# Kernel optimization log

Measured on AMD Instinct MI355X. Metric: run time of the kernel, lower is better.

Reference implementation:

```python
import jax, jax.numpy as jnp
import numpy as np

ALPHA = 0.8   # dice-score exponent
BETA = 0.2    # class-prob exponent
EPS = 1e-4    # dice denominator epsilon (SparseInst dice_score)


def _hungarian_max(cost):
    """Rectangular linear_sum_assignment(maximize=True) for a numpy (n,m) cost.
    Pads to square, runs the O(s^3) Hungarian algorithm with potentials.
    Returns (rows, cols) of length min(n,m), rows sorted (matches scipy)."""
    n, m = cost.shape
    s = max(n, m)
    c = np.zeros((s, s), dtype=np.float64)
    c[:n, :m] = -cost  # maximize -> minimize
    INF = 1e18
    u = np.zeros(s + 1)
    v = np.zeros(s + 1)
    p = np.zeros(s + 1, dtype=np.int64)
    way = np.zeros(s + 1, dtype=np.int64)
    for i in range(1, s + 1):
        p[0] = i
        j0 = 0
        minv = np.full(s + 1, INF)
        used = np.zeros(s + 1, dtype=bool)
        while True:
            used[j0] = True
            i0 = p[j0]
            cur = c[i0 - 1, :] - u[i0] - v[1:]
            free = ~used[1:]
            upd = free & (cur < minv[1:])
            minv[1:][upd] = cur[upd]
            way[1:][upd] = j0
            cand = np.where(free, minv[1:], INF)
            j1 = int(np.argmin(cand)) + 1
            delta = cand[j1 - 1]
            u[p[used]] += delta
            v[used] -= delta
            minv[~used] -= delta
            j0 = j1
            if p[j0] == 0:
                break
        while j0:
            j1 = way[j0]
            p[j0] = p[j1]
            j0 = j1
    rows, cols = [], []
    for j in range(1, s + 1):
        i = p[j]
        if i - 1 < n and j - 1 < m:
            rows.append(i - 1)
            cols.append(j - 1)
    order = np.argsort(np.asarray(rows))
    return np.asarray(rows)[order], np.asarray(cols)[order]


def _cost_matrix(pred_masks, pred_logits, tgt_masks, tgt_ids):
    B, N, H, W = pred_masks.shape
    T = tgt_masks.shape[0]
    pm = jax.nn.sigmoid(pred_masks.astype(jnp.float32)).reshape(B * N, H * W)
    # bilinear resize (align_corners=False / half-pixel) of GT masks to pred grid
    tm = jax.image.resize(tgt_masks.astype(jnp.float32), (T, H, W), method='linear')
    tm = tm.reshape(T, H * W)
    # dice score: 2<p,t> / (|p|^2 + |t|^2 + eps)   -> (B*N, T)
    num = 2.0 * jnp.einsum('qd,td->qt', pm, tm)
    den = jnp.sum(pm * pm, axis=-1)[:, None] + jnp.sum(tm * tm, axis=-1)[None, :]
    dice = num / (den + EPS)
    prob = jax.nn.sigmoid(pred_logits.astype(jnp.float32)).reshape(B * N, -1)[:, tgt_ids]
    C = dice ** ALPHA * prob ** BETA
    return C.reshape(B, N, T)


_cost_matrix_jit = jax.jit(_cost_matrix)


def setup_inputs() -> dict:
    key = jax.random.key(0)
    k1, k2, k3, k4 = jax.random.split(key, 4)
    B, N, H, W = 16, 100, 128, 128
    T, NC = 320, 80
    return {
        'pred_masks': jax.random.normal(k1, (B, N, H, W), dtype=jnp.float32),
        'pred_logits': jax.random.normal(k2, (B, N, NC), dtype=jnp.float32),
        'tgt_masks': jax.random.uniform(k3, (T, 2 * H, 2 * W), dtype=jnp.float32),
        'tgt_ids': jax.random.randint(k4, (T,), 0, NC, dtype=jnp.int64) if jax.config.jax_enable_x64 else jax.random.randint(k4, (T,), 0, NC, dtype=jnp.int32),
    }


def reference(pred_masks, pred_logits, tgt_masks, tgt_ids):
    B, N = pred_masks.shape[:2]
    T = tgt_masks.shape[0]
    per_img = T // B  # uniform sizes per image (stands in for [len(v['masks'])])
    C = _cost_matrix_jit(pred_masks, pred_logits, tgt_masks, tgt_ids)
    Cn = np.asarray(jax.device_get(C))
    rows, cols = [], []
    for b in range(B):
        r, c = _hungarian_max(Cn[b, :, b * per_img:(b + 1) * per_img])
        rows.append(r)
        cols.append(c)
    rows = jnp.asarray(np.stack(rows), dtype=jnp.int32)  # (B, per_img)
    cols = jnp.asarray(np.stack(cols), dtype=jnp.int32)  # (B, per_img)
    return C, rows, cols
```

## Files before the change

kernel.cpp:

```cpp
#include <hip/hip_runtime.h>
#include <math.h>

#define NB 16
#define NP 100
#define NT 320
#define NCLS 80
#define WO 128
#define HW 16384
#define QT 1600
#define PI 20
#define KSPLIT 8
#define KSLICE 2048
#define BK 32
#define KTILES 64
#define SRC_W 256
#define BM 32
#define BN 320
#define CH 16

typedef _Float16 half2v __attribute__((ext_vector_type(2)));
typedef _Float16 half4v __attribute__((ext_vector_type(4)));
typedef _Float16 half8v __attribute__((ext_vector_type(8)));
typedef float f32x4 __attribute__((ext_vector_type(4)));

#define GLOAD_LDS16(gp, lp) __builtin_amdgcn_global_load_lds(                         \
    (const __attribute__((address_space(1))) void*)(gp),                              \
    (__attribute__((address_space(3))) void*)(lp), 16, 0, 0)

#define SWZ(r) (((r) & 3) ^ (((r) >> 2) & 3))

__device__ __forceinline__ float sigf(float x){ return 1.0f/(1.0f+expf(-x)); }
__device__ __forceinline__ float sigfast(float x){ return 1.0f/(1.0f+__expf(-x)); }

__device__ __forceinline__ void mkw128(int i, float* w, int* ix){
  int j0 = 2*i - 1;
  ix[0]=j0; ix[1]=j0+1; ix[2]=j0+2; ix[3]=j0+3;
  w[0]=0.125f; w[1]=0.375f; w[2]=0.375f; w[3]=0.125f;
  if (i == 0){ ix[0]=0; w[0]=0.0f; w[1]=3.0f/7.0f; w[2]=3.0f/7.0f; w[3]=1.0f/7.0f; }
  if (i == 127){ ix[3]=255; w[3]=0.0f; w[0]=1.0f/7.0f; w[1]=3.0f/7.0f; w[2]=3.0f/7.0f; }
}

__global__ __launch_bounds__(256) void k_downsample(const float* __restrict__ tgt,
                                                    _Float16* __restrict__ tm,
                                                    float* __restrict__ tqpart){
  const int blk = blockIdx.x;
  const int t = blk >> 3;
  const int c = blk & 7;
  const int x = threadIdx.x;
  const int oy0 = c * CH;
  const int r0 = 2*oy0 - 1;
  const float* src = tgt + (size_t)t * (SRC_W*SRC_W);
  __shared__ float vbuf[CH][SRC_W];
  __shared__ float wred[4];

  float cc[34];
  #pragma unroll
  for (int li = 0; li < 34; ++li){
    int r = r0 + li; r = r < 0 ? 0 : (r > 255 ? 255 : r);
    cc[li] = src[r*SRC_W + x];
  }
  #pragma unroll
  for (int dy = 0; dy < CH; ++dy){
    int oy = oy0 + dy;
    float w0=0.125f, w1=0.375f, w2=0.375f, w3=0.125f;
    if (oy == 0){ w0=0.0f; w1=3.0f/7.0f; w2=3.0f/7.0f; w3=1.0f/7.0f; }
    if (oy == 127){ w3=0.0f; w0=1.0f/7.0f; w1=3.0f/7.0f; w2=3.0f/7.0f; }
    vbuf[dy][x] = w0*cc[2*dy] + w1*cc[2*dy+1] + w2*cc[2*dy+2] + w3*cc[2*dy+3];
  }
  __syncthreads();

  float ssq = 0.f;
  _Float16* dst = tm + (size_t)t * HW + (size_t)oy0 * WO;
  #pragma unroll
  for (int i = 0; i < 8; ++i){
    int e = x + 256*i;
    int oy = e >> 7;
    int ox = e & 127;
    float w[4]; int ix[4];
    mkw128(ox, w, ix);
    float val = w[0]*vbuf[oy][ix[0]] + w[1]*vbuf[oy][ix[1]]
              + w[2]*vbuf[oy][ix[2]] + w[3]*vbuf[oy][ix[3]];
    dst[oy*WO + ox] = (_Float16)val;
    ssq += val*val;
  }
  for (int off=32; off; off>>=1) ssq += __shfl_xor(ssq, off);
  if ((x & 63) == 0) wred[x >> 6] = ssq;
  __syncthreads();
  if (x == 0) tqpart[c*NT + t] = wred[0]+wred[1]+wred[2]+wred[3];
}

__global__ __launch_bounds__(512) void k_gemm(const float* __restrict__ A,
                                              const _Float16* __restrict__ Bm,
                                              float* __restrict__ part,
                                              float* __restrict__ pqpart){
  __shared__ _Float16 As[2][BM*BK];
  __shared__ _Float16 Bs[2][BN*BK];
  const int tid = threadIdx.x;
  const int lane = tid & 63;
  const int wid = tid >> 6;
  const int wr = wid & 1;
  const int wc = wid >> 1;
  const int id = blockIdx.x;
  const int z = id & 7;
  const int q0 = (id >> 3) * BM;
  const int ks = z * KSLICE;

  const int ar = tid >> 4;
  const int acg = tid & 15;
  const float* ap = A + (size_t)(q0 + ar) * HW + ks + acg*2;
  const int awoff = ar*BK + ((acg >> 2) ^ SWZ(ar))*8 + (acg & 3)*2;

  f32x4 acc[5];
  #pragma unroll
  for (int n = 0; n < 5; ++n) acc[n] = (f32x4){0.f,0.f,0.f,0.f};
  float pqs = 0.f;

  #pragma unroll
  for (int i = 0; i < 3; ++i){
    int g = i*512 + tid;
    if (g < 1280){
      int row = g >> 2, slot = g & 3;
      const _Float16* gp = Bm + (size_t)row*HW + ks + (slot ^ SWZ(row))*8;
      GLOAD_LDS16(gp, &Bs[0][(size_t)g*8]);
    }
  }
  {
    float2 a0 = *(const float2*)ap;
    float s0 = sigfast(a0.x), s1 = sigfast(a0.y);
    pqs += s0*s0 + s1*s1;
    half2v hh = { (_Float16)s0, (_Float16)s1 };
    *(half2v*)&As[0][awoff] = hh;
  }
  __syncthreads();

  for (int kt = 0; kt < KTILES; ++kt){
    const int cur = kt & 1, nxt = cur ^ 1;
    float2 a;
    if (kt + 1 < KTILES){
      #pragma unroll
      for (int i = 0; i < 3; ++i){
        int g = i*512 + tid;
        if (g < 1280){
          int row = g >> 2, slot = g & 3;
          const _Float16* gp = Bm + (size_t)row*HW + ks + (kt+1)*BK + (slot ^ SWZ(row))*8;
          GLOAD_LDS16(gp, &Bs[nxt][(size_t)g*8]);
        }
      }
      a = *(const float2*)(ap + (kt+1)*BK);
    }
    half8v af, bf[5];
    {
      int r = wr*16 + (lane & 15);
      af = *(const half8v*)&As[cur][r*BK + (((lane>>4) ^ SWZ(r)))*8];
    }
    #pragma unroll
    for (int n = 0; n < 5; ++n){
      int r = wc*80 + n*16 + (lane & 15);
      bf[n] = *(const half8v*)&Bs[cur][r*BK + (((lane>>4) ^ SWZ(r)))*8];
    }
    #pragma unroll
    for (int n = 0; n < 5; ++n)
      acc[n] = __builtin_amdgcn_mfma_f32_16x16x32_f16(af, bf[n], acc[n], 0, 0, 0);
    if (kt + 1 < KTILES){
      float s0 = sigfast(a.x), s1 = sigfast(a.y);
      pqs += s0*s0 + s1*s1;
      half2v hh = { (_Float16)s0, (_Float16)s1 };
      *(half2v*)&As[nxt][awoff] = hh;
    }
    __syncthreads();
  }

  float* op = part + (size_t)z * (QT*NT);
  {
    int qb = q0 + wr*16 + (lane >> 4)*4;
    #pragma unroll
    for (int n = 0; n < 5; ++n){
      int t = wc*80 + n*16 + (lane & 15);
      #pragma unroll
      for (int r = 0; r < 4; ++r)
        op[(size_t)(qb + r)*NT + t] = acc[n][r];
    }
  }
  pqs += __shfl_xor(pqs, 1);
  pqs += __shfl_xor(pqs, 2);
  pqs += __shfl_xor(pqs, 4);
  pqs += __shfl_xor(pqs, 8);
  if ((tid & 15) == 0) pqpart[z*QT + q0 + ar] = pqs;
}

__global__ __launch_bounds__(256) void k_cost(const float* __restrict__ part,
                                              const float* __restrict__ pqpart,
                                              const float* __restrict__ tqpart,
                                              const float* __restrict__ logits,
                                              const int* __restrict__ ids,
                                              float* __restrict__ Cout){
  int idx = blockIdx.x * 256 + threadIdx.x;
  int q = idx / NT;
  int t = idx - q * NT;
  float num = 0.f;
  #pragma unroll
  for (int s = 0; s < KSPLIT; ++s) num += part[(size_t)s * (QT*NT) + idx];
  num *= 2.0f;
  float pqv = 0.f;
  #pragma unroll
  for (int s = 0; s < KSPLIT; ++s) pqv += pqpart[s * QT + q];
  float tqv = 0.f;
  #pragma unroll
  for (int s = 0; s < 8; ++s) tqv += tqpart[s * NT + t];
  float den = pqv + tqv + 1e-4f;
  float dice = num / den;
  float prob = sigf(logits[q * NCLS + ids[t]]);
  Cout[idx] = powf(dice, 0.8f) * powf(prob, 0.2f);
}

__global__ __launch_bounds__(64) void k_hung(const float* __restrict__ C,
                                             float* __restrict__ rows_out,
                                             float* __restrict__ cols_out){
  const int b = blockIdx.x;
  const int lane = threadIdx.x;
  __shared__ float negC[PI*NP];
  __shared__ double u[PI+1];
  __shared__ int p[NP+1];
  __shared__ int way[NP+1];
  for (int e = lane; e < PI*NP; e += 64){
    int i = e / NP, j = e - i*NP;
    negC[e] = -C[(size_t)(b*NP + j)*NT + (b*PI + i)];
  }
  if (lane <= PI) u[lane] = 0.0;
  for (int j = lane; j <= NP; j += 64){ p[j] = 0; way[j] = 0; }
  __syncthreads();
  const int jA = lane + 1;
  const int jB = lane + 65;
  const bool hasB = (jB <= NP);
  double vA = 0.0, vB = 0.0;
  const double INFD = 1e18;
  for (int i = 1; i <= PI; ++i){
    if (lane == 0) p[0] = i;
    __syncthreads();
    double mvA = INFD, mvB = INFD;
    bool usA = false, usB = false;
    int j0 = 0;
    int jbrk = 0;
    while (true){
      if (jA == j0) usA = true;
      if (hasB && jB == j0) usB = true;
      int i0 = p[j0];
      double ui0 = u[i0];
      double candA = INFD, candB = INFD;
      if (!usA){
        double cur = (double)negC[(i0-1)*NP + (jA-1)] - ui0 - vA;
        if (cur < mvA){ mvA = cur; way[jA] = j0; }
        candA = mvA;
      }
      if (hasB && !usB){
        double cur = (double)negC[(i0-1)*NP + (jB-1)] - ui0 - vB;
        if (cur < mvB){ mvB = cur; way[jB] = j0; }
        candB = mvB;
      }
      double bv; int bj;
      if (candB < candA){ bv = candB; bj = jB; } else { bv = candA; bj = jA; }
      for (int off = 32; off; off >>= 1){
        double ov = __shfl_xor(bv, off);
        int oj = __shfl_xor(bj, off);
        if (ov < bv || (ov == bv && oj < bj)){ bv = ov; bj = oj; }
      }
      const double delta = bv;
      if (usA){ int pj = p[jA]; u[pj] += delta; vA -= delta; }
      else mvA -= delta;
      if (hasB){
        if (usB){ int pj = p[jB]; u[pj] += delta; vB -= delta; }
        else mvB -= delta;
      }
      if (lane == 0) u[p[0]] += delta;
      __syncthreads();
      j0 = bj;
      if (p[j0] == 0){ jbrk = j0; break; }
    }
    __syncthreads();
    if (lane == 0){
      int j0a = jbrk;
      while (j0a){
        int jp = way[j0a];
        p[j0a] = p[jp];
        j0a = jp;
      }
    }
    __syncthreads();
  }
  if (lane == 0){
    int cnt = 0;
    for (int j = 1; j <= NP; ++j){
      int pi = p[j];
      if (pi != 0){
        rows_out[b*PI + cnt] = (float)(j - 1);
        cols_out[b*PI + cnt] = (float)(pi - 1);
        ++cnt;
      }
    }
  }
}

extern "C" void kernel_launch(void* const* d_in, const int* in_sizes, int n_in,
                              void* d_out, int out_size, void* d_ws, size_t ws_size,
                              hipStream_t stream){
  const float* pred_masks  = (const float*)d_in[0];
  const float* pred_logits = (const float*)d_in[1];
  const float* tgt_masks   = (const float*)d_in[2];
  const int*   tgt_ids     = (const int*)d_in[3];
  float* out = (float*)d_out;
  char* ws = (char*)d_ws;
  _Float16* Th  = (_Float16*)ws;
  float* tqpart = (float*)(ws + (size_t)NT*HW*2);
  float* pqpart = (float*)(ws + (size_t)NT*HW*2 + 16384);
  float* part   = (float*)(ws + (size_t)NT*HW*2 + 16384 + 65536);

  k_downsample<<<NT*8, 256, 0, stream>>>(tgt_masks, Th, tqpart);
  k_gemm<<<50*KSPLIT, 512, 0, stream>>>(pred_masks, Th, part, pqpart);
  k_cost<<<(QT*NT)/256, 256, 0, stream>>>(part, pqpart, tqpart, pred_logits, tgt_ids, out);
  k_hung<<<NB, 64, 0, stream>>>(out, out + (size_t)QT*NT, out + (size_t)QT*NT + NT);
}
```

Measured before the change: 138.2 us.

## Load GEMM A operand directly into registers and double the K tile

```diff
diff --git a/kernel.cpp b/kernel.cpp
--- a/kernel.cpp
+++ b/kernel.cpp
@@ -11,23 +11,19 @@
 #define PI 20
 #define KSPLIT 8
 #define KSLICE 2048
-#define BK 32
-#define KTILES 64
+#define BK 64
+#define KTILES 32
 #define SRC_W 256
 #define BM 32
 #define BN 320
 #define CH 16
 
-typedef _Float16 half2v __attribute__((ext_vector_type(2)));
-typedef _Float16 half4v __attribute__((ext_vector_type(4)));
 typedef _Float16 half8v __attribute__((ext_vector_type(8)));
 typedef float f32x4 __attribute__((ext_vector_type(4)));
 
 #define GLOAD_LDS16(gp, lp) __builtin_amdgcn_global_load_lds(                         \
     (const __attribute__((address_space(1))) void*)(gp),                              \
     (__attribute__((address_space(3))) void*)(lp), 16, 0, 0)
-
-#define SWZ(r) (((r) & 3) ^ (((r) >> 2) & 3))
 
 __device__ __forceinline__ float sigf(float x){ return 1.0f/(1.0f+expf(-x)); }
 __device__ __forceinline__ float sigfast(float x){ return 1.0f/(1.0f+__expf(-x)); }
@@ -89,26 +85,22 @@
   if (x == 0) tqpart[c*NT + t] = wred[0]+wred[1]+wred[2]+wred[3];
 }
 
-__global__ __launch_bounds__(512) void k_gemm(const float* __restrict__ A,
-                                              const _Float16* __restrict__ Bm,
-                                              float* __restrict__ part,
-                                              float* __restrict__ pqpart){
-  __shared__ _Float16 As[2][BM*BK];
+__global__ __launch_bounds__(512, 3) void k_gemm(const float* __restrict__ A,
+                                                 const _Float16* __restrict__ Bm,
+                                                 float* __restrict__ part,
+                                                 float* __restrict__ pqpart){
   __shared__ _Float16 Bs[2][BN*BK];
   const int tid = threadIdx.x;
   const int lane = tid & 63;
   const int wid = tid >> 6;
-  const int wr = wid & 1;
-  const int wc = wid >> 1;
+  const int wr = wid >> 2;
+  const int wc = wid & 3;
   const int id = blockIdx.x;
   const int z = id & 7;
   const int q0 = (id >> 3) * BM;
   const int ks = z * KSLICE;
 
-  const int ar = tid >> 4;
-  const int acg = tid & 15;
-  const float* ap = A + (size_t)(q0 + ar) * HW + ks + acg*2;
-  const int awoff = ar*BK + ((acg >> 2) ^ SWZ(ar))*8 + (acg & 3)*2;
+  const float* ap = A + (size_t)(q0 + wr*16 + (lane & 15)) * HW + ks + (lane >> 4) * 8;
 
   f32x4 acc[5];
   #pragma unroll
@@ -116,58 +108,68 @@
   float pqs = 0.f;
 
   #pragma unroll
-  for (int i = 0; i < 3; ++i){
+  for (int i = 0; i < 5; ++i){
     int g = i*512 + tid;
-    if (g < 1280){
-      int row = g >> 2, slot = g & 3;
-      const _Float16* gp = Bm + (size_t)row*HW + ks + (slot ^ SWZ(row))*8;
-      GLOAD_LDS16(gp, &Bs[0][(size_t)g*8]);
-    }
-  }
-  {
-    float2 a0 = *(const float2*)ap;
-    float s0 = sigfast(a0.x), s1 = sigfast(a0.y);
-    pqs += s0*s0 + s1*s1;
-    half2v hh = { (_Float16)s0, (_Float16)s1 };
-    *(half2v*)&As[0][awoff] = hh;
-  }
-  __syncthreads();
+    int row = g >> 3, s = g & 7;
+    GLOAD_LDS16(Bm + (size_t)row*HW + ks + ((s ^ (row & 7)) * 8), &Bs[0][(size_t)g*8]);
+  }
+  float4 a0 = *(const float4*)(ap);
+  float4 a1 = *(const float4*)(ap + 4);
+  float4 a2 = *(const float4*)(ap + 32);
+  float4 a3 = *(const float4*)(ap + 36);
+  asm volatile("s_waitcnt vmcnt(0)" ::: "memory");
+  __builtin_amdgcn_s_barrier();
 
   for (int kt = 0; kt < KTILES; ++kt){
     const int cur = kt & 1, nxt = cur ^ 1;
-    float2 a;
     if (kt + 1 < KTILES){
       #pragma unroll
-      for (int i = 0; i < 3; ++i){
+      for (int i = 0; i < 5; ++i){
         int g = i*512 + tid;
-        if (g < 1280){
-          int row = g >> 2, slot = g & 3;
-          const _Float16* gp = Bm + (size_t)row*HW + ks + (kt+1)*BK + (slot ^ SWZ(row))*8;
-          GLOAD_LDS16(gp, &Bs[nxt][(size_t)g*8]);
-        }
-      }
-      a = *(const float2*)(ap + (kt+1)*BK);
-    }
-    half8v af, bf[5];
+        int row = g >> 3, s = g & 7;
+        GLOAD_LDS16(Bm + (size_t)row*HW + ks + (kt+1)*BK + ((s ^ (row & 7)) * 8),
+                    &Bs[nxt][(size_t)g*8]);
+      }
+    }
+    float4 b0, b1, b2, b3;
+    if (kt + 1 < KTILES){
+      const float* apn = ap + (kt+1)*BK;
+      b0 = *(const float4*)(apn);
+      b1 = *(const float4*)(apn + 4);
+      b2 = *(const float4*)(apn + 32);
+      b3 = *(const float4*)(apn + 36);
+    }
     {
-      int r = wr*16 + (lane & 15);
-      af = *(const half8v*)&As[cur][r*BK + (((lane>>4) ^ SWZ(r)))*8];
-    }
-    #pragma unroll
-    for (int n = 0; n < 5; ++n){
-      int r = wc*80 + n*16 + (lane & 15);
-      bf[n] = *(const half8v*)&Bs[cur][r*BK + (((lane>>4) ^ SWZ(r)))*8];
-    }
-    #pragma unroll
-    for (int n = 0; n < 5; ++n)
-      acc[n] = __builtin_amdgcn_mfma_f32_16x16x32_f16(af, bf[n], acc[n], 0, 0, 0);
-    if (kt + 1 < KTILES){
-      float s0 = sigfast(a.x), s1 = sigfast(a.y);
-      pqs += s0*s0 + s1*s1;
-      half2v hh = { (_Float16)s0, (_Float16)s1 };
-      *(half2v*)&As[nxt][awoff] = hh;
-    }
-    __syncthreads();
+      float s0 = sigfast(a0.x), s1 = sigfast(a0.y), s2 = sigfast(a0.z), s3 = sigfast(a0.w);
+      float s4 = sigfast(a1.x), s5 = sigfast(a1.y), s6 = sigfast(a1.z), s7 = sigfast(a1.w);
+      pqs += s0*s0 + s1*s1 + s2*s2 + s3*s3 + s4*s4 + s5*s5 + s6*s6 + s7*s7;
+      half8v af = { (_Float16)s0, (_Float16)s1, (_Float16)s2, (_Float16)s3,
+                    (_Float16)s4, (_Float16)s5, (_Float16)s6, (_Float16)s7 };
+      #pragma unroll
+      for (int n = 0; n < 5; ++n){
+        int r = wc*80 + n*16 + (lane & 15);
+        int s = 0*4 + (lane >> 4);
+        half8v bf = *(const half8v*)&Bs[cur][r*BK + ((s ^ (r & 7)) * 8)];
+        acc[n] = __builtin_amdgcn_mfma_f32_16x16x32_f16(af, bf, acc[n], 0, 0, 0);
+      }
+    }
+    {
+      float s0 = sigfast(a2.x), s1 = sigfast(a2.y), s2 = sigfast(a2.z), s3 = sigfast(a2.w);
+      float s4 = sigfast(a3.x), s5 = sigfast(a3.y), s6 = sigfast(a3.z), s7 = sigfast(a3.w);
+      pqs += s0*s0 + s1*s1 + s2*s2 + s3*s3 + s4*s4 + s5*s5 + s6*s6 + s7*s7;
+      half8v af = { (_Float16)s0, (_Float16)s1, (_Float16)s2, (_Float16)s3,
+                    (_Float16)s4, (_Float16)s5, (_Float16)s6, (_Float16)s7 };
+      #pragma unroll
+      for (int n = 0; n < 5; ++n){
+        int r = wc*80 + n*16 + (lane & 15);
+        int s = 1*4 + (lane >> 4);
+        half8v bf = *(const half8v*)&Bs[cur][r*BK + ((s ^ (r & 7)) * 8)];
+        acc[n] = __builtin_amdgcn_mfma_f32_16x16x32_f16(af, bf, acc[n], 0, 0, 0);
+      }
+    }
+    asm volatile("s_waitcnt vmcnt(4)" ::: "memory");
+    __builtin_amdgcn_s_barrier();
+    if (kt + 1 < KTILES){ a0 = b0; a1 = b1; a2 = b2; a3 = b3; }
   }
 
   float* op = part + (size_t)z * (QT*NT);
@@ -181,11 +183,11 @@
         op[(size_t)(qb + r)*NT + t] = acc[n][r];
     }
   }
-  pqs += __shfl_xor(pqs, 1);
-  pqs += __shfl_xor(pqs, 2);
-  pqs += __shfl_xor(pqs, 4);
-  pqs += __shfl_xor(pqs, 8);
-  if ((tid & 15) == 0) pqpart[z*QT + q0 + ar] = pqs;
+  if (wc == 0){
+    pqs += __shfl_xor(pqs, 16);
+    pqs += __shfl_xor(pqs, 32);
+    if (lane < 16) pqpart[z*QT + q0 + wr*16 + lane] = pqs;
+  }
 }
 
 __global__ __launch_bounds__(256) void k_cost(const float* __restrict__ part,
```

After: 156.0 us. 1.13x slower.

## Retile split-K GEMM to 64x160 blocks with BK=64 and deeper A prefetch

Applied to the files above, without the earlier changes.

```diff
diff --git a/kernel.cpp b/kernel.cpp
--- a/kernel.cpp
+++ b/kernel.cpp
@@ -11,23 +11,19 @@
 #define PI 20
 #define KSPLIT 8
 #define KSLICE 2048
-#define BK 32
-#define KTILES 64
+#define BK 64
+#define KTILES 32
 #define SRC_W 256
-#define BM 32
-#define BN 320
+#define BM 64
+#define BN 160
 #define CH 16
 
-typedef _Float16 half2v __attribute__((ext_vector_type(2)));
-typedef _Float16 half4v __attribute__((ext_vector_type(4)));
 typedef _Float16 half8v __attribute__((ext_vector_type(8)));
 typedef float f32x4 __attribute__((ext_vector_type(4)));
 
 #define GLOAD_LDS16(gp, lp) __builtin_amdgcn_global_load_lds(                         \
     (const __attribute__((address_space(1))) void*)(gp),                              \
     (__attribute__((address_space(3))) void*)(lp), 16, 0, 0)
-
-#define SWZ(r) (((r) & 3) ^ (((r) >> 2) & 3))
 
 __device__ __forceinline__ float sigf(float x){ return 1.0f/(1.0f+expf(-x)); }
 __device__ __forceinline__ float sigfast(float x){ return 1.0f/(1.0f+__expf(-x)); }
@@ -89,26 +85,26 @@
   if (x == 0) tqpart[c*NT + t] = wred[0]+wred[1]+wred[2]+wred[3];
 }
 
-__global__ __launch_bounds__(512) void k_gemm(const float* __restrict__ A,
-                                              const _Float16* __restrict__ Bm,
-                                              float* __restrict__ part,
-                                              float* __restrict__ pqpart){
+__global__ __launch_bounds__(512, 4) void k_gemm(const float* __restrict__ A,
+                                                 const _Float16* __restrict__ Bm,
+                                                 float* __restrict__ part,
+                                                 float* __restrict__ pqpart){
   __shared__ _Float16 As[2][BM*BK];
   __shared__ _Float16 Bs[2][BN*BK];
   const int tid = threadIdx.x;
   const int lane = tid & 63;
   const int wid = tid >> 6;
-  const int wr = wid & 1;
-  const int wc = wid >> 1;
-  const int id = blockIdx.x;
-  const int z = id & 7;
-  const int q0 = (id >> 3) * BM;
+  const int rg = wid >> 1;
+  const int cg = wid & 1;
+  const int q0 = blockIdx.x * BM;
+  const int t0 = blockIdx.y * BN;
+  const int z  = blockIdx.z;
   const int ks = z * KSLICE;
 
-  const int ar = tid >> 4;
-  const int acg = tid & 15;
-  const float* ap = A + (size_t)(q0 + ar) * HW + ks + acg*2;
-  const int awoff = ar*BK + ((acg >> 2) ^ SWZ(ar))*8 + (acg & 3)*2;
+  const int ar = tid >> 3;
+  const int ac8 = tid & 7;
+  const float* ap = A + (size_t)(q0 + ar) * HW + ks + ac8*8;
+  const int awoff = ar*BK + ((ac8 ^ (ar & 7)) * 8);
 
   f32x4 acc[5];
   #pragma unroll
@@ -119,73 +115,97 @@
   for (int i = 0; i < 3; ++i){
     int g = i*512 + tid;
     if (g < 1280){
-      int row = g >> 2, slot = g & 3;
-      const _Float16* gp = Bm + (size_t)row*HW + ks + (slot ^ SWZ(row))*8;
-      GLOAD_LDS16(gp, &Bs[0][(size_t)g*8]);
+      int row = g >> 3, s = g & 7;
+      GLOAD_LDS16(Bm + (size_t)(t0 + row)*HW + ks + ((s ^ (row & 7)) * 8),
+                  &Bs[0][(size_t)g*8]);
     }
   }
   {
-    float2 a0 = *(const float2*)ap;
-    float s0 = sigfast(a0.x), s1 = sigfast(a0.y);
-    pqs += s0*s0 + s1*s1;
-    half2v hh = { (_Float16)s0, (_Float16)s1 };
-    *(half2v*)&As[0][awoff] = hh;
-  }
-  __syncthreads();
+    float4 v0 = *(const float4*)(ap);
+    float4 v1 = *(const float4*)(ap + 4);
+    float s0 = sigfast(v0.x), s1 = sigfast(v0.y), s2 = sigfast(v0.z), s3 = sigfast(v0.w);
+    float s4 = sigfast(v1.x), s5 = sigfast(v1.y), s6 = sigfast(v1.z), s7 = sigfast(v1.w);
+    pqs += s0*s0 + s1*s1 + s2*s2 + s3*s3 + s4*s4 + s5*s5 + s6*s6 + s7*s7;
+    half8v hh = { (_Float16)s0, (_Float16)s1, (_Float16)s2, (_Float16)s3,
+                  (_Float16)s4, (_Float16)s5, (_Float16)s6, (_Float16)s7 };
+    *(half8v*)&As[0][awoff] = hh;
+  }
+  float4 aCur0 = *(const float4*)(ap + BK);
+  float4 aCur1 = *(const float4*)(ap + BK + 4);
+  asm volatile("s_waitcnt vmcnt(2) lgkmcnt(0)" ::: "memory");
+  __builtin_amdgcn_s_barrier();
 
   for (int kt = 0; kt < KTILES; ++kt){
     const int cur = kt & 1, nxt = cur ^ 1;
-    float2 a;
     if (kt + 1 < KTILES){
       #pragma unroll
       for (int i = 0; i < 3; ++i){
         int g = i*512 + tid;
         if (g < 1280){
-          int row = g >> 2, slot = g & 3;
-          const _Float16* gp = Bm + (size_t)row*HW + ks + (kt+1)*BK + (slot ^ SWZ(row))*8;
-          GLOAD_LDS16(gp, &Bs[nxt][(size_t)g*8]);
+          int row = g >> 3, s = g & 7;
+          GLOAD_LDS16(Bm + (size_t)(t0 + row)*HW + ks + (kt+1)*BK + ((s ^ (row & 7)) * 8),
+                      &Bs[nxt][(size_t)g*8]);
         }
       }
-      a = *(const float2*)(ap + (kt+1)*BK);
-    }
-    half8v af, bf[5];
-    {
-      int r = wr*16 + (lane & 15);
-      af = *(const half8v*)&As[cur][r*BK + (((lane>>4) ^ SWZ(r)))*8];
-    }
+    }
+    float4 aNext0, aNext1;
+    if (kt + 2 < KTILES){
+      const float* apn = ap + (kt+2)*BK;
+      aNext0 = *(const float4*)(apn);
+      aNext1 = *(const float4*)(apn + 4);
+    }
+    #pragma unroll
+    for (int s = 0; s < 2; ++s){
+      half8v af, bf[5];
+      {
+        int r = rg*16 + (lane & 15);
+        int c = s*4 + (lane >> 4);
+        af = *(const half8v*)&As[cur][r*BK + ((c ^ (r & 7)) * 8)];
+      }
+      #pragma unroll
+      for (int n = 0; n < 5; ++n){
+        int r = cg*80 + n*16 + (lane & 15);
+        int c = s*4 + (lane >> 4);
+        bf[n] = *(const half8v*)&Bs[cur][r*BK + ((c ^ (r & 7)) * 8)];
+      }
+      #pragma unroll
+      for (int n = 0; n < 5; ++n)
+        acc[n] = __builtin_amdgcn_mfma_f32_16x16x32_f16(af, bf[n], acc[n], 0, 0, 0);
+    }
+    if (kt + 1 < KTILES){
+      float s0 = sigfast(aCur0.x), s1 = sigfast(aCur0.y), s2 = sigfast(aCur0.z), s3 = sigfast(aCur0.w);
+      float s4 = sigfast(aCur1.x), s5 = sigfast(aCur1.y), s6 = sigfast(aCur1.z), s7 = sigfast(aCur1.w);
+      pqs += s0*s0 + s1*s1 + s2*s2 + s3*s3 + s4*s4 + s5*s5 + s6*s6 + s7*s7;
+      half8v hh = { (_Float16)s0, (_Float16)s1, (_Float16)s2, (_Float16)s3,
+                    (_Float16)s4, (_Float16)s5, (_Float16)s6, (_Float16)s7 };
+      *(half8v*)&As[nxt][awoff] = hh;
+      aCur0 = aNext0; aCur1 = aNext1;
+    }
+    if (kt + 2 < KTILES){
+      asm volatile("s_waitcnt vmcnt(2) lgkmcnt(0)" ::: "memory");
+    } else {
+      asm volatile("s_waitcnt vmcnt(0) lgkmcnt(0)" ::: "memory");
+    }
+    __builtin_amdgcn_s_barrier();
+  }
+
+  float* op = part + (size_t)z * (QT*NT);
+  {
+    int qb = q0 + rg*16 + (lane >> 4)*4;
     #pragma unroll
     for (int n = 0; n < 5; ++n){
-      int r = wc*80 + n*16 + (lane & 15);
-      bf[n] = *(const half8v*)&Bs[cur][r*BK + (((lane>>4) ^ SWZ(r)))*8];
-    }
-    #pragma unroll
-    for (int n = 0; n < 5; ++n)
-      acc[n] = __builtin_amdgcn_mfma_f32_16x16x32_f16(af, bf[n], acc[n], 0, 0, 0);
-    if (kt + 1 < KTILES){
-      float s0 = sigfast(a.x), s1 = sigfast(a.y);
-      pqs += s0*s0 + s1*s1;
-      half2v hh = { (_Float16)s0, (_Float16)s1 };
-      *(half2v*)&As[nxt][awoff] = hh;
-    }
-    __syncthreads();
-  }
-
-  float* op = part + (size_t)z * (QT*NT);
-  {
-    int qb = q0 + wr*16 + (lane >> 4)*4;
-    #pragma unroll
-    for (int n = 0; n < 5; ++n){
-      int t = wc*80 + n*16 + (lane & 15);
+      int t = t0 + cg*80 + n*16 + (lane & 15);
       #pragma unroll
       for (int r = 0; r < 4; ++r)
         op[(size_t)(qb + r)*NT + t] = acc[n][r];
     }
   }
-  pqs += __shfl_xor(pqs, 1);
-  pqs += __shfl_xor(pqs, 2);
-  pqs += __shfl_xor(pqs, 4);
-  pqs += __shfl_xor(pqs, 8);
-  if ((tid & 15) == 0) pqpart[z*QT + q0 + ar] = pqs;
+  if (blockIdx.y == 0){
+    pqs += __shfl_xor(pqs, 1);
+    pqs += __shfl_xor(pqs, 2);
+    pqs += __shfl_xor(pqs, 4);
+    if ((tid & 7) == 0) pqpart[z*QT + q0 + ar] = pqs;
+  }
 }
 
 __global__ __launch_bounds__(256) void k_cost(const float* __restrict__ part,
@@ -315,7 +335,8 @@
   float* part   = (float*)(ws + (size_t)NT*HW*2 + 16384 + 65536);
 
   k_downsample<<<NT*8, 256, 0, stream>>>(tgt_masks, Th, tqpart);
-  k_gemm<<<50*KSPLIT, 512, 0, stream>>>(pred_masks, Th, part, pqpart);
+  dim3 g(QT/BM, NT/BN, KSPLIT);
+  k_gemm<<<g, 512, 0, stream>>>(pred_masks, Th, part, pqpart);
   k_cost<<<(QT*NT)/256, 256, 0, stream>>>(part, pqpart, tqpart, pred_logits, tgt_ids, out);
   k_hung<<<NB, 64, 0, stream>>>(out, out + (size_t)QT*NT, out + (size_t)QT*NT + NT);
 }
```

New measurement: 125.8 us. 1.1x faster.
